# Performance work log

Measured on AMD Instinct MI355X. Metric: run time of the kernel, lower is better.

## Reference

```python
import jax, jax.numpy as jnp
import numpy as np

# Bit-slice configuration from the module defaults: slices [1,1,2,4] -> 8-bit signed INT.
# The crossbar engine's MapReduceDot decomposes the quantized integers into bit-planes,
# runs partial dot products per (input-slice, weight-slice) pair across paral_size
# partitions, and recombines them with 2^shift weights. In the ideal (noise-free)
# engine this recombination is EXACT, so the forward math equals:
#   dequant(blockwise_quant(x)) @ dequant(blockwise_quant(W^T)) + bias
# with per-block scales determined by the quant granularities.
IN_BITS = 1 + 1 + 2 + 4   # sum(input_slice)  = 8
W_BITS = 1 + 1 + 2 + 4    # sum(weight_slice) = 8
IN_GRAN = (1, 32)         # (rows, cols) blocks over (seq, in_features)
W_GRAN = (32, 32)         # blocks over (in_features, out_features) of weight.t()


def block_fake_quant(x, bits, gran):
    """Symmetric per-block fake quantization (quantize -> dequantize).

    x: [..., R, C]; gran=(gr, gc) tiles the last two dims. Each (gr, gc) block
    gets its own max-abs scale, matching SlicedData's quant_gran semantics.
    """
    qmax = float(2 ** (bits - 1) - 1)  # 127 for 8-bit
    gr, gc = gran
    lead = x.shape[:-2]
    R, C = x.shape[-2], x.shape[-1]
    xb = x.reshape(*lead, R // gr, gr, C // gc, gc)
    mx = jnp.max(jnp.abs(xb), axis=(-3, -1), keepdims=True)
    scale = jnp.where(mx > 0, mx / qmax, jnp.ones_like(mx))
    q = jnp.clip(jnp.round(xb / scale), -qmax, qmax) * scale
    return q.reshape(x.shape)


def setup_inputs() -> dict:
    key = jax.random.key(0)
    k1, k2, k3 = jax.random.split(key, 3)
    B, S, Din, Dout = 4, 4096, 2048, 2048
    x = jax.random.normal(k1, (B, S, Din), dtype=jnp.float32)
    # kaiming_uniform_(a=sqrt(5)) on a Linear weight is U(-1/sqrt(fan_in), 1/sqrt(fan_in))
    bound = 1.0 / np.sqrt(Din)
    weight = jax.random.uniform(k2, (Dout, Din), jnp.float32, -bound, bound)
    bias = jax.random.uniform(k3, (Dout,), jnp.float32, -bound, bound)
    return {"x": x, "weight": weight, "bias": bias}


def reference(x, weight, bias):
    # Quantize activations per (1, 32) block and weight.t() per (32, 32) block,
    # then recombine via the (mathematically exact) bit-sliced dot == dense GEMM
    # on the dequantized values.
    qx = block_fake_quant(x, IN_BITS, IN_GRAN)            # [B, S, Din]
    qw = block_fake_quant(weight.T, W_BITS, W_GRAN)       # [Din, Dout]
    out = jnp.einsum('bsd,de->bse', qx, qw) + bias        # [B, S, Dout]
    return out
```

## Files before the change

kernel.cpp:

```cpp
#include <hip/hip_runtime.h>
#include <hip/hip_bf16.h>
#include <stdint.h>

#define M_TOT 16384
#define N_TOT 2048
#define K_TOT 2048
#define NT 32

typedef __attribute__((ext_vector_type(8))) short bf16x8;
typedef __attribute__((ext_vector_type(4))) float f32x4;

__device__ __forceinline__ ushort f32_to_bf16_rne(float f) {
    uint32_t u = __float_as_uint(f);
    uint32_t r = (u + 0x7fffu + ((u >> 16) & 1u)) >> 16;
    return (ushort)r;
}

__device__ __forceinline__ void async_copy16(const void* gptr, void* lptr) {
    __builtin_amdgcn_global_load_lds(
        (const __attribute__((address_space(1))) uint32_t*)gptr,
        (__attribute__((address_space(3))) uint32_t*)lptr,
        16, 0, 0);
}

__global__ void quant_x_kernel(const float* __restrict__ x, ushort* __restrict__ qx) {
    const int tid = blockIdx.x * 256 + threadIdx.x;
    const float4 v = ((const float4*)x)[tid];
    float m = fmaxf(fmaxf(fabsf(v.x), fabsf(v.y)), fmaxf(fabsf(v.z), fabsf(v.w)));
    m = fmaxf(m, __shfl_xor(m, 1));
    m = fmaxf(m, __shfl_xor(m, 2));
    m = fmaxf(m, __shfl_xor(m, 4));
    const float s = (m > 0.f) ? (m / 127.f) : 1.f;
    const float q0 = fminf(fmaxf(rintf(v.x / s), -127.f), 127.f) * s;
    const float q1 = fminf(fmaxf(rintf(v.y / s), -127.f), 127.f) * s;
    const float q2 = fminf(fmaxf(rintf(v.z / s), -127.f), 127.f) * s;
    const float q3 = fminf(fmaxf(rintf(v.w / s), -127.f), 127.f) * s;
    ushort4 r;
    r.x = f32_to_bf16_rne(q0);
    r.y = f32_to_bf16_rne(q1);
    r.z = f32_to_bf16_rne(q2);
    r.w = f32_to_bf16_rne(q3);
    ((ushort4*)qx)[tid] = r;
}

__global__ void quant_w_kernel(const float* __restrict__ w, ushort* __restrict__ qw) {
    const int gtid = blockIdx.x * 256 + threadIdx.x;
    const int wid  = gtid >> 6;
    const int lane = gtid & 63;
    const int tn = wid >> 6;
    const int tk = wid & 63;
    const int row = tn * 32 + (lane >> 1);
    const int col = tk * 32 + ((lane & 1) << 4);
    const float* p = w + (size_t)row * K_TOT + col;
    const float4 v0 = ((const float4*)p)[0];
    const float4 v1 = ((const float4*)p)[1];
    const float4 v2 = ((const float4*)p)[2];
    const float4 v3 = ((const float4*)p)[3];
    float m = 0.f;
#define MAX4(V) m = fmaxf(m, fmaxf(fmaxf(fabsf(V.x), fabsf(V.y)), fmaxf(fabsf(V.z), fabsf(V.w))));
    MAX4(v0) MAX4(v1) MAX4(v2) MAX4(v3)
#undef MAX4
    #pragma unroll
    for (int off = 1; off < 64; off <<= 1) m = fmaxf(m, __shfl_xor(m, off));
    const float s = (m > 0.f) ? (m / 127.f) : 1.f;
    float vv[16] = {v0.x, v0.y, v0.z, v0.w, v1.x, v1.y, v1.z, v1.w,
                    v2.x, v2.y, v2.z, v2.w, v3.x, v3.y, v3.z, v3.w};
    union { ushort us[16]; uint4 q[2]; } o;
    #pragma unroll
    for (int i = 0; i < 16; ++i) {
        const float q = fminf(fmaxf(rintf(vv[i] / s), -127.f), 127.f) * s;
        o.us[i] = f32_to_bf16_rne(q);
    }
    uint4* dst = (uint4*)(qw + (size_t)row * K_TOT + col);
    dst[0] = o.q[0];
    dst[1] = o.q[1];
}

#define LDSA(tb, row, colus) \
    (*(const bf16x8*)&As[tb][row][(colus) ^ (((row) & 7) << 3)])
#define LDSB(tb, row, colus) \
    (*(const bf16x8*)&Bs[tb][row][(colus) ^ (((row) & 7) << 3)])

#define STAGE_A(tb, hh, li, tt)                                                          \
    async_copy16(Agbase + (size_t)((hh) * 128 + (li) * 64) * K_TOT + (size_t)(tt) * 64,  \
                 (char*)&As[0][0][0] + (tb) * 32768 + (hh) * 16384 + (li) * 8192 + (wv << 10));
#define STAGE_B(tb, hh, li, tt)                                                          \
    async_copy16(Bgbase + (size_t)((hh) * 128 + (li) * 64) * K_TOT + (size_t)(tt) * 64,  \
                 (char*)&Bs[0][0][0] + (tb) * 32768 + (hh) * 16384 + (li) * 8192 + (wv << 10));
#define STAGE_A2(tb, hh, tt)  { STAGE_A(tb, hh, 0, tt) STAGE_A(tb, hh, 1, tt) }
#define STAGE_B2(tb, hh, tt)  { STAGE_B(tb, hh, 0, tt) STAGE_B(tb, hh, 1, tt) }

#define WAITLGKM4 { asm volatile("s_waitcnt lgkmcnt(4)" ::: "memory"); __builtin_amdgcn_sched_barrier(0); }
#define WAITLGKM0 { asm volatile("s_waitcnt lgkmcnt(0)" ::: "memory"); __builtin_amdgcn_sched_barrier(0); }

#define RD_AF(DST, tb, q) {                                   \
    DST[0] = LDSA(tb, ab + (q) * 32,      h8);                \
    DST[1] = LDSA(tb, ab + (q) * 32,      32 + h8);           \
    DST[2] = LDSA(tb, ab + (q) * 32 + 16, h8);                \
    DST[3] = LDSA(tb, ab + (q) * 32 + 16, 32 + h8); }

#define RD_BG(tb) {                                                           \
    _Pragma("unroll")                                                         \
    for (int j = 0; j < 4; ++j) {                                             \
        const int bb = wcn * 64 + j * 16 + r;                                 \
        bg[j][0] = LDSB(tb, bb, h8);  bg[j][1] = LDSB(tb, bb, 32 + h8);       \
    } }

#define MFMA_PH(i0, AF)                                                                   \
    __builtin_amdgcn_s_setprio(1);                                                        \
    _Pragma("unroll")                                                                     \
    for (int j = 0; j < 4; ++j) {                                                         \
        acc[i0][j]     = __builtin_amdgcn_mfma_f32_16x16x32_bf16(AF[0], bg[j][0], acc[i0][j], 0, 0, 0);     \
        acc[i0][j]     = __builtin_amdgcn_mfma_f32_16x16x32_bf16(AF[1], bg[j][1], acc[i0][j], 0, 0, 0);     \
        acc[(i0)+1][j] = __builtin_amdgcn_mfma_f32_16x16x32_bf16(AF[2], bg[j][0], acc[(i0)+1][j], 0, 0, 0); \
        acc[(i0)+1][j] = __builtin_amdgcn_mfma_f32_16x16x32_bf16(AF[3], bg[j][1], acc[(i0)+1][j], 0, 0, 0); \
    }                                                                                     \
    __builtin_amdgcn_s_setprio(0);

#define TILE_BODY(tb, t, STA, STB, RDBG, VM1, VM3)                                        \
  {                                                                                       \
                      \
    RD_AF(afX, tb, 0)                                                                     \
    __builtin_amdgcn_sched_barrier(0);                                                    \
    RD_AF(afY, tb, 1)                                                                     \
    if (STA) STAGE_A2(tb ^ 1, 0, (t) + 1)                                                 \
    WAITLGKM4                                                                             \
    MFMA_PH(0, afX)                                                                       \
                  \
    RD_AF(afX, tb, 2)                                                                     \
    if (STA) STAGE_A2(tb ^ 1, 1, (t) + 1)                                                 \
    WAITLGKM4                                                                             \
    MFMA_PH(2, afY)                                                                       \
    if ((VM1) == 4) { asm volatile("s_waitcnt vmcnt(4)" ::: "memory"); }                  \
    else if ((VM1) == 0) { asm volatile("s_waitcnt vmcnt(0)" ::: "memory"); }             \
    __builtin_amdgcn_s_barrier();         \
                                  \
    RD_AF(afY, tb, 3)                                                                     \
    if (STB) STAGE_B2(tb, 0, (t) + 2)                                                     \
    WAITLGKM4                                                                             \
    MFMA_PH(4, afX)                                                                       \
                  \
    if (STB) STAGE_B2(tb, 1, (t) + 2)                                                     \
    WAITLGKM0                                                                             \
    MFMA_PH(6, afY)                                                                       \
    if (RDBG) RD_BG((tb) ^ 1)               \
    if ((VM3) == 4) { asm volatile("s_waitcnt vmcnt(4)" ::: "memory"); }                  \
    else if ((VM3) == 0) { asm volatile("s_waitcnt vmcnt(0)" ::: "memory"); }             \
    __builtin_amdgcn_s_barrier();                        \
  }

__global__ __launch_bounds__(512, 2) void gemm_pipe4_kernel(
    const ushort* __restrict__ A,
    const ushort* __restrict__ Bt,
    const float* __restrict__ bias,
    float* __restrict__ C) {

    __shared__ ushort As[2][256][64];
    __shared__ ushort Bs[2][256][64];

    const int tid  = threadIdx.x;
    const int lane = tid & 63;
    const int wv   = tid >> 6;
    const int wmr  = wv >> 2;
    const int wcn  = wv & 3;
    const int r    = lane & 15;
    const int h8   = (lane >> 4) << 3;

    const int nbn  = N_TOT / 256;
    const int nwg  = (M_TOT / 256) * nbn;
    const int cpx  = nwg >> 3;
    const int swz  = (blockIdx.x & 7) * cpx + (blockIdx.x >> 3);
    const int brow = (swz / nbn) * 256;
    const int bcol = (swz % nbn) * 256;

    const int srow = tid >> 3;
    const int scol = (((tid & 7) ^ (srow & 7)) << 3);
    const ushort* Agbase = A  + (size_t)(brow + srow) * K_TOT + scol;
    const ushort* Bgbase = Bt + (size_t)(bcol + srow) * K_TOT + scol;

    const int ab = wmr * 128 + r;

    f32x4 acc[8][4];
    const f32x4 zero = {0.f, 0.f, 0.f, 0.f};
    #pragma unroll
    for (int i = 0; i < 8; ++i)
        #pragma unroll
        for (int j = 0; j < 4; ++j) acc[i][j] = zero;

    STAGE_A2(0, 0, 0) STAGE_A2(0, 1, 0)
    STAGE_B2(0, 0, 0) STAGE_B2(0, 1, 0)
    STAGE_B2(1, 0, 1) STAGE_B2(1, 1, 1)
    asm volatile("s_waitcnt vmcnt(4)" ::: "memory");
    __builtin_amdgcn_s_barrier();

    bf16x8 afX[4], afY[4];
    bf16x8 bg[4][2];
    RD_BG(0)
    __builtin_amdgcn_sched_barrier(0);

    for (int t = 0; t < NT - 2; t += 2) {
        TILE_BODY(0, t,     1, 1, 1, 4, 4)
        TILE_BODY(1, t + 1, 1, 1, 1, 4, 4)
    }
    TILE_BODY(0, NT - 2, 1, 0, 1, 4, 0)
    TILE_BODY(1, NT - 1, 0, 0, 0, -1, -1)

    const int hq = (lane >> 4) * 4;
    float bv[4];
    #pragma unroll
    for (int j = 0; j < 4; ++j) bv[j] = bias[bcol + wcn * 64 + j * 16 + r];
    #pragma unroll
    for (int i = 0; i < 8; ++i) {
        const int row0 = brow + wmr * 128 + i * 16 + hq;
        #pragma unroll
        for (int j = 0; j < 4; ++j) {
            const int col = bcol + wcn * 64 + j * 16 + r;
            #pragma unroll
            for (int jj = 0; jj < 4; ++jj)
                C[(size_t)(row0 + jj) * N_TOT + col] = acc[i][j][jj] + bv[j];
        }
    }
}

extern "C" void kernel_launch(void* const* d_in, const int* in_sizes, int n_in,
                              void* d_out, int out_size, void* d_ws, size_t ws_size,
                              hipStream_t stream) {
    const float* x    = (const float*)d_in[0];
    const float* wgt  = (const float*)d_in[1];
    const float* bias = (const float*)d_in[2];
    float* out = (float*)d_out;

    ushort* qx = (ushort*)d_ws;
    ushort* qw = qx + (size_t)M_TOT * K_TOT;

    quant_x_kernel<<<(M_TOT * K_TOT / 4) / 256, 256, 0, stream>>>(x, qx);
    quant_w_kernel<<<(64 * 64 * 64) / 256, 256, 0, stream>>>(wgt, qw);
    gemm_pipe4_kernel<<<(M_TOT / 256) * (N_TOT / 256), 512, 0, stream>>>(qx, qw, bias, out);
}
```

Measured before the change: 170.4 us.

## Triple-buffer B tiles in LDS to drop the mid-tile barrier

Grows the B shared-memory buffer from two to three slots and rotates the read and write slots across K iterations. This lets each tile keep only one workgroup barrier instead of two, and B fragments are now read at the start of each tile instead of at the end of the previous one. The aim is to cut synchronization stalls between the MFMA phases. In exchange, LDS use rises to 160KB per block and slot indices become runtime values. The B reads also have less time to hide their latency before the first MFMA phase.

```diff
diff --git a/kernel.cpp b/kernel.cpp
--- a/kernel.cpp
+++ b/kernel.cpp
@@ -78,17 +78,17 @@
 
 #define LDSA(tb, row, colus) \
     (*(const bf16x8*)&As[tb][row][(colus) ^ (((row) & 7) << 3)])
-#define LDSB(tb, row, colus) \
-    (*(const bf16x8*)&Bs[tb][row][(colus) ^ (((row) & 7) << 3)])
+#define LDSB(slot, row, colus) \
+    (*(const bf16x8*)&Bs[slot][row][(colus) ^ (((row) & 7) << 3)])
 
 #define STAGE_A(tb, hh, li, tt)                                                          \
     async_copy16(Agbase + (size_t)((hh) * 128 + (li) * 64) * K_TOT + (size_t)(tt) * 64,  \
                  (char*)&As[0][0][0] + (tb) * 32768 + (hh) * 16384 + (li) * 8192 + (wv << 10));
-#define STAGE_B(tb, hh, li, tt)                                                          \
+#define STAGE_B(slot, hh, li, tt)                                                        \
     async_copy16(Bgbase + (size_t)((hh) * 128 + (li) * 64) * K_TOT + (size_t)(tt) * 64,  \
-                 (char*)&Bs[0][0][0] + (tb) * 32768 + (hh) * 16384 + (li) * 8192 + (wv << 10));
-#define STAGE_A2(tb, hh, tt)  { STAGE_A(tb, hh, 0, tt) STAGE_A(tb, hh, 1, tt) }
-#define STAGE_B2(tb, hh, tt)  { STAGE_B(tb, hh, 0, tt) STAGE_B(tb, hh, 1, tt) }
+                 (char*)&Bs[0][0][0] + (size_t)(slot) * 32768 + (hh) * 16384 + (li) * 8192 + (wv << 10));
+#define STAGE_A2(tb, hh, tt)    { STAGE_A(tb, hh, 0, tt) STAGE_A(tb, hh, 1, tt) }
+#define STAGE_B2(slot, hh, tt)  { STAGE_B(slot, hh, 0, tt) STAGE_B(slot, hh, 1, tt) }
 
 #define WAITLGKM4 { asm volatile("s_waitcnt lgkmcnt(4)" ::: "memory"); __builtin_amdgcn_sched_barrier(0); }
 #define WAITLGKM0 { asm volatile("s_waitcnt lgkmcnt(0)" ::: "memory"); __builtin_amdgcn_sched_barrier(0); }
@@ -99,11 +99,11 @@
     DST[2] = LDSA(tb, ab + (q) * 32 + 16, h8);                \
     DST[3] = LDSA(tb, ab + (q) * 32 + 16, 32 + h8); }
 
-#define RD_BG(tb) {                                                           \
+#define RD_BG(slot) {                                                         \
     _Pragma("unroll")                                                         \
     for (int j = 0; j < 4; ++j) {                                             \
         const int bb = wcn * 64 + j * 16 + r;                                 \
-        bg[j][0] = LDSB(tb, bb, h8);  bg[j][1] = LDSB(tb, bb, 32 + h8);       \
+        bg[j][0] = LDSB(slot, bb, h8);  bg[j][1] = LDSB(slot, bb, 32 + h8);   \
     } }
 
 #define MFMA_PH(i0, AF)                                                                   \
@@ -117,46 +117,42 @@
     }                                                                                     \
     __builtin_amdgcn_s_setprio(0);
 
-#define TILE_BODY(tb, t, STA, STB, RDBG, VM1, VM3)                                        \
+#define TILE_BODY(tb, t, STA, STB, VMC, BRD, BWR)                                         \
   {                                                                                       \
-                      \
+                   \
     RD_AF(afX, tb, 0)                                                                     \
-    __builtin_amdgcn_sched_barrier(0);                                                    \
+    RD_BG(BRD)                                                                            \
     RD_AF(afY, tb, 1)                                                                     \
     if (STA) STAGE_A2(tb ^ 1, 0, (t) + 1)                                                 \
     WAITLGKM4                                                                             \
     MFMA_PH(0, afX)                                                                       \
-                  \
+                                        \
     RD_AF(afX, tb, 2)                                                                     \
     if (STA) STAGE_A2(tb ^ 1, 1, (t) + 1)                                                 \
     WAITLGKM4                                                                             \
     MFMA_PH(2, afY)                                                                       \
-    if ((VM1) == 4) { asm volatile("s_waitcnt vmcnt(4)" ::: "memory"); }                  \
-    else if ((VM1) == 0) { asm volatile("s_waitcnt vmcnt(0)" ::: "memory"); }             \
-    __builtin_amdgcn_s_barrier();         \
-                                  \
+                     \
     RD_AF(afY, tb, 3)                                                                     \
-    if (STB) STAGE_B2(tb, 0, (t) + 2)                                                     \
+    if (STB) STAGE_B2(BWR, 0, (t) + 2)                                                    \
     WAITLGKM4                                                                             \
     MFMA_PH(4, afX)                                                                       \
-                  \
-    if (STB) STAGE_B2(tb, 1, (t) + 2)                                                     \
+                    \
+    if (STB) STAGE_B2(BWR, 1, (t) + 2)                                                    \
     WAITLGKM0                                                                             \
     MFMA_PH(6, afY)                                                                       \
-    if (RDBG) RD_BG((tb) ^ 1)               \
-    if ((VM3) == 4) { asm volatile("s_waitcnt vmcnt(4)" ::: "memory"); }                  \
-    else if ((VM3) == 0) { asm volatile("s_waitcnt vmcnt(0)" ::: "memory"); }             \
-    __builtin_amdgcn_s_barrier();                        \
+    if ((VMC) == 4)      { asm volatile("s_waitcnt vmcnt(4)" ::: "memory"); }             \
+    else if ((VMC) == 0) { asm volatile("s_waitcnt vmcnt(0)" ::: "memory"); }             \
+    __builtin_amdgcn_s_barrier();          \
   }
 
-__global__ __launch_bounds__(512, 2) void gemm_pipe4_kernel(
+__global__ __launch_bounds__(512, 2) void gemm_pipe5_kernel(
     const ushort* __restrict__ A,
     const ushort* __restrict__ Bt,
     const float* __restrict__ bias,
     float* __restrict__ C) {
 
     __shared__ ushort As[2][256][64];
-    __shared__ ushort Bs[2][256][64];
+    __shared__ ushort Bs[3][256][64];
 
     const int tid  = threadIdx.x;
     const int lane = tid & 63;
@@ -195,15 +191,19 @@
 
     bf16x8 afX[4], afY[4];
     bf16x8 bg[4][2];
-    RD_BG(0)
-    __builtin_amdgcn_sched_barrier(0);
+
+    int brd = 0;
+    int bwr = 2;
 
     for (int t = 0; t < NT - 2; t += 2) {
-        TILE_BODY(0, t,     1, 1, 1, 4, 4)
-        TILE_BODY(1, t + 1, 1, 1, 1, 4, 4)
+        TILE_BODY(0, t,     1, 1, 4, brd, bwr)
+        brd = (brd == 2) ? 0 : brd + 1;  bwr = (bwr == 2) ? 0 : bwr + 1;
+        TILE_BODY(1, t + 1, 1, 1, 4, brd, bwr)
+        brd = (brd == 2) ? 0 : brd + 1;  bwr = (bwr == 2) ? 0 : bwr + 1;
     }
-    TILE_BODY(0, NT - 2, 1, 0, 1, 4, 0)
-    TILE_BODY(1, NT - 1, 0, 0, 0, -1, -1)
+    TILE_BODY(0, NT - 2, 1, 0, 0, brd, 0)
+    brd = (brd == 2) ? 0 : brd + 1;
+    TILE_BODY(1, NT - 1, 0, 0, -1, brd, 0)
 
     const int hq = (lane >> 4) * 4;
     float bv[4];
@@ -235,5 +235,5 @@
 
     quant_x_kernel<<<(M_TOT * K_TOT / 4) / 256, 256, 0, stream>>>(x, qx);
     quant_w_kernel<<<(64 * 64 * 64) / 256, 256, 0, stream>>>(wgt, qw);
-    gemm_pipe4_kernel<<<(M_TOT / 256) * (N_TOT / 256), 512, 0, stream>>>(qx, qw, bias, out);
-}
+    gemm_pipe5_kernel<<<(M_TOT / 256) * (N_TOT / 256), 512, 0, stream>>>(qx, qw, bias, out);
+}
```

New measurement: 165.3 us. -3.0%, faster.
